# Optimization experiments

Hardware: AMD Instinct MI355X
Metric: run time of the kernel (lower is better)

Reference implementation:

```python
import jax, jax.numpy as jnp
import numpy as np

# 3D PGA grade slices over the 16-component multivector (contiguous in standard basis order)
GRADE_SLICES = [(0, 1), (1, 5), (5, 11), (11, 15), (15, 16)]
GRADE_DIMS = [1, 4, 6, 4, 1]


def setup_inputs() -> dict:
    key = jax.random.key(0)
    ks = jax.random.split(key, 11)
    x = jax.random.normal(ks[0], (8, 2048, 128, 16), dtype=jnp.float32)
    inp = {"x": x}
    for g, d in enumerate(GRADE_DIMS):
        # match nn.Linear default init scale ~ U(-1/sqrt(d), 1/sqrt(d)); randn is fine for a numeric baseline
        inp[f"w{g}"] = jax.random.normal(ks[1 + 2 * g], (d, d), dtype=jnp.float32) / np.sqrt(d)
        inp[f"b{g}"] = jax.random.normal(ks[2 + 2 * g], (d,), dtype=jnp.float32) / np.sqrt(d)
    return inp


def reference(x, w0, b0, w1, b1, w2, b2, w3, b3, w4, b4):
    ws = [w0, w1, w2, w3, w4]
    bs = [b0, b1, b2, b3, b4]
    # Block-diagonal per-grade linear: gather slice, y = x_g @ W_g^T + b_g, scatter back.
    # Since grade index sets are contiguous, scatter == concatenate along last dim.
    outs = []
    for (lo, hi), w, b in zip(GRADE_SLICES, ws, bs):
        xg = x[..., lo:hi]                       # [..., d_g]
        outs.append(jnp.einsum("...i,oi->...o", xg, w) + b)
    return jnp.concatenate(outs, axis=-1)        # [..., 16]
```

## Files before the change

### kernel.cpp

```cpp
#include <hip/hip_runtime.h>


__global__ __launch_bounds__(256) void GradeWiseLinear_kernel(
    const float* __restrict__ x,
    const float* __restrict__ w0, const float* __restrict__ b0,
    const float* __restrict__ w1, const float* __restrict__ b1,
    const float* __restrict__ w2, const float* __restrict__ b2,
    const float* __restrict__ w3, const float* __restrict__ b3,
    const float* __restrict__ w4, const float* __restrict__ b4,
    float* __restrict__ out, int n_rows)
{
    __shared__ float s[86];
    {
        int t = threadIdx.x;
        if (t < 86) {
            float v;
            if      (t == 0)  v = w0[0];
            else if (t < 17)  v = w1[t - 1];
            else if (t < 53)  v = w2[t - 17];
            else if (t < 69)  v = w3[t - 53];
            else if (t == 69) v = w4[0];
            else if (t == 70) v = b0[0];
            else if (t < 75)  v = b1[t - 71];
            else if (t < 81)  v = b2[t - 75];
            else if (t < 85)  v = b3[t - 81];
            else              v = b4[0];
            s[t] = v;
        }
    }
    __syncthreads();

    long r = (long)blockIdx.x * blockDim.x + threadIdx.x;
    if (r >= n_rows) return;

    const float4* xv = (const float4*)x + r * 4;
    float4 a0 = xv[0];
    float4 a1 = xv[1];
    float4 a2 = xv[2];
    float4 a3 = xv[3];
    float in[16] = {a0.x, a0.y, a0.z, a0.w,
                    a1.x, a1.y, a1.z, a1.w,
                    a2.x, a2.y, a2.z, a2.w,
                    a3.x, a3.y, a3.z, a3.w};
    float o[16];

    o[0] = s[70] + in[0] * s[0];

    #pragma unroll
    for (int oo = 0; oo < 4; ++oo) {
        float acc = s[71 + oo];
        #pragma unroll
        for (int i = 0; i < 4; ++i) acc += in[1 + i] * s[1 + oo * 4 + i];
        o[1 + oo] = acc;
    }

    #pragma unroll
    for (int oo = 0; oo < 6; ++oo) {
        float acc = s[75 + oo];
        #pragma unroll
        for (int i = 0; i < 6; ++i) acc += in[5 + i] * s[17 + oo * 6 + i];
        o[5 + oo] = acc;
    }

    #pragma unroll
    for (int oo = 0; oo < 4; ++oo) {
        float acc = s[81 + oo];
        #pragma unroll
        for (int i = 0; i < 4; ++i) acc += in[11 + i] * s[53 + oo * 4 + i];
        o[11 + oo] = acc;
    }

    o[15] = s[85] + in[15] * s[69];

    float4* ov = (float4*)out + r * 4;
    ov[0] = make_float4(o[0],  o[1],  o[2],  o[3]);
    ov[1] = make_float4(o[4],  o[5],  o[6],  o[7]);
    ov[2] = make_float4(o[8],  o[9],  o[10], o[11]);
    ov[3] = make_float4(o[12], o[13], o[14], o[15]);
}

extern "C" void kernel_launch(void* const* d_in, const int* in_sizes, int n_in,
                              void* d_out, int out_size, void* d_ws, size_t ws_size,
                              hipStream_t stream) {
    const float* x  = (const float*)d_in[0];
    const float* w0 = (const float*)d_in[1];
    const float* b0 = (const float*)d_in[2];
    const float* w1 = (const float*)d_in[3];
    const float* b1 = (const float*)d_in[4];
    const float* w2 = (const float*)d_in[5];
    const float* b2 = (const float*)d_in[6];
    const float* w3 = (const float*)d_in[7];
    const float* b3 = (const float*)d_in[8];
    const float* w4 = (const float*)d_in[9];
    const float* b4 = (const float*)d_in[10];
    float* out = (float*)d_out;

    int n_rows = in_sizes[0] / 16;
    int block = 256;
    int grid = (n_rows + block - 1) / block;

    GradeWiseLinear_kernel<<<grid, block, 0, stream>>>(
        x, w0, b0, w1, b1, w2, b2, w3, b3, w4, b4, out, n_rows);
}
```

Measured before the change: 252.9 us.

## Assign one float4 per thread with neighbor loads for coalesced access

```diff
diff --git a/kernel.cpp b/kernel.cpp
--- a/kernel.cpp
+++ b/kernel.cpp
@@ -8,7 +8,7 @@
     const float* __restrict__ w2, const float* __restrict__ b2,
     const float* __restrict__ w3, const float* __restrict__ b3,
     const float* __restrict__ w4, const float* __restrict__ b4,
-    float* __restrict__ out, int n_rows)
+    float* __restrict__ out, int n4)
 {
     __shared__ float s[86];
     {
@@ -30,53 +30,47 @@
     }
     __syncthreads();
 
-    long r = (long)blockIdx.x * blockDim.x + threadIdx.x;
-    if (r >= n_rows) return;
+    int g = blockIdx.x * 256 + threadIdx.x;
+    if (g >= n4) return;
 
-    const float4* xv = (const float4*)x + r * 4;
-    float4 a0 = xv[0];
-    float4 a1 = xv[1];
-    float4 a2 = xv[2];
-    float4 a3 = xv[3];
-    float in[16] = {a0.x, a0.y, a0.z, a0.w,
-                    a1.x, a1.y, a1.z, a1.w,
-                    a2.x, a2.y, a2.z, a2.w,
-                    a3.x, a3.y, a3.z, a3.w};
-    float o[16];
+    const int j = g & 3;
+    const float4* x4 = (const float4*)x;
 
-    o[0] = s[70] + in[0] * s[0];
+    float4 me = x4[g];
+    float4 up = x4[g - (int)(j > 0)];
+    float4 dn = x4[g + (int)(j < 3)];
 
-    #pragma unroll
-    for (int oo = 0; oo < 4; ++oo) {
-        float acc = s[71 + oo];
-        #pragma unroll
-        for (int i = 0; i < 4; ++i) acc += in[1 + i] * s[1 + oo * 4 + i];
-        o[1 + oo] = acc;
+    float o0, o1, o2, o3;
+
+    if (j == 0) {
+        o0 = s[70] + me.x * s[0];
+        o1 = s[71] + me.y * s[1] + me.z * s[2]  + me.w * s[3]  + dn.x * s[4];
+        o2 = s[72] + me.y * s[5] + me.z * s[6]  + me.w * s[7]  + dn.x * s[8];
+        o3 = s[73] + me.y * s[9] + me.z * s[10] + me.w * s[11] + dn.x * s[12];
+    } else if (j == 1) {
+        o0 = s[74] + up.y * s[13] + up.z * s[14] + up.w * s[15] + me.x * s[16];
+        o1 = s[75] + me.y * s[17] + me.z * s[18] + me.w * s[19]
+                   + dn.x * s[20] + dn.y * s[21] + dn.z * s[22];
+        o2 = s[76] + me.y * s[23] + me.z * s[24] + me.w * s[25]
+                   + dn.x * s[26] + dn.y * s[27] + dn.z * s[28];
+        o3 = s[77] + me.y * s[29] + me.z * s[30] + me.w * s[31]
+                   + dn.x * s[32] + dn.y * s[33] + dn.z * s[34];
+    } else if (j == 2) {
+        o0 = s[78] + up.y * s[35] + up.z * s[36] + up.w * s[37]
+                   + me.x * s[38] + me.y * s[39] + me.z * s[40];
+        o1 = s[79] + up.y * s[41] + up.z * s[42] + up.w * s[43]
+                   + me.x * s[44] + me.y * s[45] + me.z * s[46];
+        o2 = s[80] + up.y * s[47] + up.z * s[48] + up.w * s[49]
+                   + me.x * s[50] + me.y * s[51] + me.z * s[52];
+        o3 = s[81] + me.w * s[53] + dn.x * s[54] + dn.y * s[55] + dn.z * s[56];
+    } else {
+        o0 = s[82] + up.w * s[57] + me.x * s[58] + me.y * s[59] + me.z * s[60];
+        o1 = s[83] + up.w * s[61] + me.x * s[62] + me.y * s[63] + me.z * s[64];
+        o2 = s[84] + up.w * s[65] + me.x * s[66] + me.y * s[67] + me.z * s[68];
+        o3 = s[85] + me.w * s[69];
     }
 
-    #pragma unroll
-    for (int oo = 0; oo < 6; ++oo) {
-        float acc = s[75 + oo];
-        #pragma unroll
-        for (int i = 0; i < 6; ++i) acc += in[5 + i] * s[17 + oo * 6 + i];
-        o[5 + oo] = acc;
-    }
-
-    #pragma unroll
-    for (int oo = 0; oo < 4; ++oo) {
-        float acc = s[81 + oo];
-        #pragma unroll
-        for (int i = 0; i < 4; ++i) acc += in[11 + i] * s[53 + oo * 4 + i];
-        o[11 + oo] = acc;
-    }
-
-    o[15] = s[85] + in[15] * s[69];
-
-    float4* ov = (float4*)out + r * 4;
-    ov[0] = make_float4(o[0],  o[1],  o[2],  o[3]);
-    ov[1] = make_float4(o[4],  o[5],  o[6],  o[7]);
-    ov[2] = make_float4(o[8],  o[9],  o[10], o[11]);
-    ov[3] = make_float4(o[12], o[13], o[14], o[15]);
+    ((float4*)out)[g] = make_float4(o0, o1, o2, o3);
 }
 
 extern "C" void kernel_launch(void* const* d_in, const int* in_sizes, int n_in,
@@ -95,10 +89,10 @@
     const float* b4 = (const float*)d_in[10];
     float* out = (float*)d_out;
 
-    int n_rows = in_sizes[0] / 16;
+    int n4 = in_sizes[0] / 4;
     int block = 256;
-    int grid = (n_rows + block - 1) / block;
+    int grid = (n4 + block - 1) / block;
 
     GradeWiseLinear_kernel<<<grid, block, 0, stream>>>(
-        x, w0, b0, w1, b1, w2, b2, w3, b3, w4, b4, out, n_rows);
+        x, w0, b0, w1, b1, w2, b2, w3, b3, w4, b4, out, n4);
 }
```

New measurement: 245.8 us. 1.03x faster.
